# Performance work log

Measured on AMD Instinct MI355X. Metric: run time of the kernel, lower is better.

## Reference

```python
import jax, jax.numpy as jnp
import numpy as np

STRIDES = (8, 16, 32)
H = W = 640
SCORE_T = 0.5
NMS_T = 0.4


def setup_inputs() -> dict:
    key = jax.random.key(0)
    ks = jax.random.split(key, 9)
    feats = [(H // s) * (W // s) for s in STRIDES]  # 6400, 1600, 400
    d = {}
    for i, n in enumerate(feats):
        d[f"score{i}"] = jax.random.normal(ks[i], (1, n, 1), jnp.float32)
        d[f"bbox{i}"] = jax.random.normal(ks[3 + i], (1, n, 4), jnp.float32)
        d[f"kps{i}"] = jax.random.normal(ks[6 + i], (1, n, 10), jnp.float32)
    return d


def _anchors(stride):
    fh, fw = H // stride, W // stride
    yv, xv = jnp.meshgrid(jnp.arange(fh), jnp.arange(fw), indexing="ij")
    return jnp.stack([xv, yv], -1).reshape(-1, 2).astype(jnp.float32) * stride


def _decode(score, bbox, kps, stride):
    pts = _anchors(stride)                      # [N,2]
    s = jax.nn.sigmoid(score[0]).reshape(-1)    # [N]
    d = bbox[0] * stride                        # [N,4]
    x1 = pts[:, 0] - d[:, 0]
    y1 = pts[:, 1] - d[:, 1]
    x2 = pts[:, 0] + d[:, 2]
    y2 = pts[:, 1] + d[:, 3]
    b = jnp.stack([x1, y1, x2, y2], -1)         # [N,4]
    kd = (kps[0] * stride).reshape(-1, 5, 2)    # [N,5,2] (px,py pairs)
    k = (pts[:, None, :] + kd).reshape(-1, 10)  # [N,10]
    return s, b, k


def _iou(b):
    area = (b[:, 2] - b[:, 0]) * (b[:, 3] - b[:, 1])
    lt = jnp.maximum(b[:, None, :2], b[None, :, :2])
    rb = jnp.minimum(b[:, None, 2:], b[None, :, 2:])
    wh = jnp.clip(rb - lt, 0.0)
    inter = wh[..., 0] * wh[..., 1]
    return inter / (area[:, None] + area[None, :] - inter + 1e-9)


def _nms_keep(iou, valid, thresh):
    # greedy NMS on score-sorted boxes: keep i iff no earlier kept j has IoU>thresh
    n = valid.shape[0]
    def body(keep, xs):
        i, row = xs
        suppressed = jnp.any(keep & (row > thresh))
        keep = keep.at[i].set(valid[i] & ~suppressed)
        return keep, None
    keep, _ = jax.lax.scan(body, jnp.zeros(n, bool), (jnp.arange(n), iou))
    return keep


def reference(score0, score1, score2, bbox0, bbox1, bbox2, kps0, kps1, kps2):
    parts = [
        _decode(s, b, k, st)
        for s, b, k, st in zip(
            (score0, score1, score2), (bbox0, bbox1, bbox2), (kps0, kps1, kps2), STRIDES
        )
    ]
    scores = jnp.concatenate([p[0] for p in parts])  # [8400]
    boxes = jnp.concatenate([p[1] for p in parts])   # [8400,4]
    kpss = jnp.concatenate([p[2] for p in parts])    # [8400,10]
    order = jnp.argsort(-scores)                     # score-descending (NMS order)
    scores = scores[order]
    boxes = boxes[order]
    kpss = kpss[order]
    valid = scores > SCORE_T                         # threshold mask
    iou = _iou(jax.lax.stop_gradient(boxes))         # [8400,8400] ~282MB
    keep = _nms_keep(iou, valid, NMS_T)
    m = keep.astype(boxes.dtype)
    # fixed-shape equivalent of dynamic gather: suppressed rows zeroed, keep mask returned
    return boxes * m[:, None], scores * m, kpss * m[:, None], keep
```

## Files before the change

kernel.cpp:

```cpp
#include <hip/hip_runtime.h>
#include <math.h>

#define N_TOT 8400
#define MASK_WORDS 132
#define CAP 32
#define RT 33

typedef unsigned long long u64;

__device__ __forceinline__ unsigned mono_u32(float f) {
    unsigned u = __float_as_uint(f);
    return (u & 0x80000000u) ? ~u : (u | 0x80000000u);
}

__global__ void decode_kernel(const float* __restrict__ score0, const float* __restrict__ bbox0, const float* __restrict__ kps0,
                              const float* __restrict__ score1, const float* __restrict__ bbox1, const float* __restrict__ kps1,
                              const float* __restrict__ score2, const float* __restrict__ bbox2, const float* __restrict__ kps2,
                              float* __restrict__ logit, float* __restrict__ sig,
                              float* __restrict__ box, float* __restrict__ kps,
                              u64* __restrict__ key, int* __restrict__ rank,
                              unsigned int* __restrict__ cnt,
                              u64* __restrict__ validw, u64* __restrict__ rowflag) {
    int i = blockIdx.x * blockDim.x + threadIdx.x;
    if (i >= N_TOT) return;
    if (i < MASK_WORDS) { validw[i] = 0ull; rowflag[i] = 0ull; }
    rank[i] = 0;
    cnt[i] = 0u;
    const float *sc, *bb, *kp;
    int m, F; float s;
    if (i < 6400)      { sc = score0; bb = bbox0; kp = kps0; m = i;        F = 80; s = 8.f;  }
    else if (i < 8000) { sc = score1; bb = bbox1; kp = kps1; m = i - 6400; F = 40; s = 16.f; }
    else               { sc = score2; bb = bbox2; kp = kps2; m = i - 8000; F = 20; s = 32.f; }
    float px = (float)(m % F) * s;
    float py = (float)(m / F) * s;
    float lg = sc[m];
    logit[i] = lg;
    sig[i] = 1.0f / (1.0f + expf(-lg));
    key[i] = ((u64)(~mono_u32(lg)) << 14) | (u64)i;
    float d0 = bb[m*4+0]*s, d1 = bb[m*4+1]*s, d2 = bb[m*4+2]*s, d3 = bb[m*4+3]*s;
    box[i*4+0] = px - d0;
    box[i*4+1] = py - d1;
    box[i*4+2] = px + d2;
    box[i*4+3] = py + d3;
    #pragma unroll
    for (int c = 0; c < 5; ++c) {
        kps[i*10 + 2*c]   = px + kp[m*10 + 2*c]   * s;
        kps[i*10 + 2*c+1] = py + kp[m*10 + 2*c+1] * s;
    }
}

__global__ __launch_bounds__(256) void rank_kernel(const u64* __restrict__ key, int* __restrict__ rank) {
    __shared__ u64 tile[256];
    int i = blockIdx.x * 256 + threadIdx.x;
    int t0 = blockIdx.y * 256;
    u64 ki = (i < N_TOT) ? key[i] : 0ull;
    int j = t0 + threadIdx.x;
    tile[threadIdx.x] = (j < N_TOT) ? key[j] : ~0ull;
    __syncthreads();
    if (i >= N_TOT) return;
    int rk = 0;
    #pragma unroll 8
    for (int k = 0; k < 256; ++k) {
        rk += (tile[k] < ki) ? 1 : 0;
    }
    if (rk) atomicAdd(&rank[i], rk);
}

__global__ void scatter_kernel(const int* __restrict__ rank,
                               const float* __restrict__ logit, const float* __restrict__ sig,
                               const float* __restrict__ box, const float* __restrict__ kps,
                               float* __restrict__ s_logit, float* __restrict__ s_sig,
                               float* __restrict__ s_box, float* __restrict__ s_kps,
                               u64* __restrict__ validw) {
    int i = blockIdx.x * blockDim.x + threadIdx.x;
    if (i >= N_TOT) return;
    int r = rank[i];
    float lg = logit[i];
    s_logit[r] = lg;
    s_sig[r] = sig[i];
    #pragma unroll
    for (int c = 0; c < 4; ++c)  s_box[r*4+c] = box[i*4+c];
    #pragma unroll
    for (int c = 0; c < 10; ++c) s_kps[r*10+c] = kps[i*10+c];
    if (lg > 0.f) atomicOr(&validw[r >> 6], 1ull << (r & 63));
}

__global__ __launch_bounds__(64) void pairs_kernel(const float* __restrict__ s_logit,
                                                   const float* __restrict__ s_box,
                                                   unsigned int* __restrict__ cnt,
                                                   ulonglong2* __restrict__ ent,
                                                   u64* __restrict__ rowflag) {
    int x = blockIdx.x;
    int y = blockIdx.y;
    int rb, cw;
    if (x + y < MASK_WORDS) { rb = x; cw = x + y; }
    else {
        if (y == MASK_WORDS / 2) return;
        rb = x + y - MASK_WORDS; cw = x;
    }
    int tid = threadIdx.x;

    __shared__ float4 cbox[64];
    __shared__ float  carea[64];
    int j0 = cw * 64;
    int j = j0 + tid;
    float4 cb = make_float4(0.f, 0.f, 0.f, 0.f);
    float lgj = -1.f;
    if (j < N_TOT) {
        cb = ((const float4*)s_box)[j];
        lgj = s_logit[j];
    }
    cbox[tid] = cb;
    carea[tid] = (cb.z - cb.x) * (cb.w - cb.y);
    u64 cvalid = __ballot(j < N_TOT && lgj > 0.f);
    __syncthreads();
    if (cvalid == 0ull) return;

    int r = rb * 64 + tid;
    float lgr = (r < N_TOT) ? s_logit[r] : -1.f;
    if (__ballot(lgr > 0.f) == 0ull) return;

    u64 bits = 0ull;
    if (lgr > 0.f) {
        float4 rb4 = ((const float4*)s_box)[r];
        float rarea = (rb4.z - rb4.x) * (rb4.w - rb4.y);
        #pragma unroll 4
        for (int k = 0; k < 64; ++k) {
            float4 c4 = cbox[k];
            float ltx = fmaxf(rb4.x, c4.x);
            float lty = fmaxf(rb4.y, c4.y);
            float rbx = fminf(rb4.z, c4.z);
            float rby = fminf(rb4.w, c4.w);
            float w = fmaxf(rbx - ltx, 0.f);
            float h = fmaxf(rby - lty, 0.f);
            float inter = w * h;
            float iou = inter / (rarea + carea[k] - inter + 1e-9f);
            bits |= (iou > 0.4f) ? (1ull << k) : 0ull;
        }
        u64 m = cvalid;
        if (cw == rb) m &= (tid == 63) ? 0ull : (~0ull << (tid + 1));
        bits &= m;
    }
    if (bits) {
        unsigned idx = atomicAdd(&cnt[r], 1u);
        if (idx < CAP) {
            ulonglong2 e; e.x = bits; e.y = (u64)cw;
            ent[(size_t)r * CAP + idx] = e;
        }
        atomicOr(&rowflag[r >> 6], 1ull << (r & 63));
    }
}

__global__ __launch_bounds__(64) void nms_kernel(const u64* __restrict__ rowflag_g,
                                                 const u64* __restrict__ validw_g,
                                                 const unsigned int* __restrict__ cnt_g,
                                                 const ulonglong2* __restrict__ ent_g,
                                                 u64* __restrict__ keep_words) {
    __shared__ u64 rem_lds[MASK_WORDS];
    __shared__ unsigned short wlist[MASK_WORDS];
    int lane = threadIdx.x;

    u64 rf[3], vw[3];
    #pragma unroll
    for (int s = 0; s < 3; ++s) {
        int w = s * 64 + lane;
        rf[s] = (w < MASK_WORDS) ? rowflag_g[w] : 0ull;
        vw[s] = (w < MASK_WORDS) ? validw_g[w] : 0ull;
        if (w < MASK_WORDS) rem_lds[w] = 0ull;
    }

    int base = 0;
    #pragma unroll
    for (int s = 0; s < 3; ++s) {
        bool nz = rf[s] != 0ull;
        u64 bal = __ballot(nz);
        int pos = __popcll(bal & ((1ull << lane) - 1ull));
        if (nz) wlist[base + pos] = (unsigned short)(s * 64 + lane);
        base += (int)__popcll(bal);
    }
    int n_w = base;
    __syncthreads();

    auto LOADW = [&](int t, int &wd, unsigned &c, ulonglong2 &e0, ulonglong2 &e1, u64 &lb) {
        wd = 0; c = 0u; e0.x = 0ull; e0.y = 0ull; e1.x = 0ull; e1.y = 0ull; lb = 0ull;
        if (t < n_w) {
            wd = (int)wlist[t];
            int row = wd * 64 + lane;
            if (row < N_TOT) {
                c = cnt_g[row];
                if (c > 0u) { e0 = ent_g[(size_t)row * CAP];     if ((int)e0.y == wd) lb |= e0.x; }
                if (c > 1u) { e1 = ent_g[(size_t)row * CAP + 1]; if ((int)e1.y == wd) lb |= e1.x; }
                if (c > 2u) {
                    unsigned cm = min(c, (unsigned)CAP);
                    for (unsigned e = 2; e < cm; ++e) {
                        ulonglong2 g = ent_g[(size_t)row * CAP + e];
                        if ((int)g.y == wd) lb |= g.x;
                    }
                }
            }
        }
    };

    int wA, wB; unsigned cA, cB; ulonglong2 eA0, eA1, eB0, eB1; u64 lbA, lbB;
    LOADW(0, wA, cA, eA0, eA1, lbA);
    LOADW(1, wB, cB, eB0, eB1, lbB);

    for (int t = 0; t < n_w; ++t) {
        int wC; unsigned cC; ulonglong2 eC0, eC1; u64 lbC;
        LOADW(t + 2, wC, cC, eC0, eC1, lbC);

        __syncthreads();
        u64 remw = rem_lds[wA];
        u64 cand = __ballot(cA > 0u) & ~remw;
        if (cand) {
            u64 kept;
            u64 localmask = __ballot(lbA != 0ull) & cand;
            if (localmask == 0ull) {
                kept = cand;
            } else {
                kept = 0ull;
                u64 remw_new = remw;
                u64 pend = cand;
                while (pend) {
                    int b = __builtin_ctzll(pend);
                    pend &= pend - 1ull;
                    if (!((remw_new >> b) & 1ull)) {
                        kept |= 1ull << b;
                        unsigned lo = (unsigned)__builtin_amdgcn_readlane((int)(unsigned)lbA, b);
                        unsigned hi = (unsigned)__builtin_amdgcn_readlane((int)(unsigned)(lbA >> 32), b);
                        remw_new |= ((u64)hi << 32) | (u64)lo;
                        pend &= ~remw_new;
                    }
                }
                if (lane == 0) rem_lds[wA] = remw_new;
            }
            if ((kept >> lane) & 1ull) {
                if (cA > 0u) { int yw = (int)eA0.y; if (yw != wA) atomicOr(&rem_lds[yw], eA0.x); }
                if (cA > 1u) { int yw = (int)eA1.y; if (yw != wA) atomicOr(&rem_lds[yw], eA1.x); }
                if (cA > 2u) {
                    unsigned cm = min(cA, (unsigned)CAP);
                    int row = wA * 64 + lane;
                    for (unsigned e = 2; e < cm; ++e) {
                        ulonglong2 g = ent_g[(size_t)row * CAP + e];
                        int yw = (int)g.y;
                        if (yw != wA) atomicOr(&rem_lds[yw], g.x);
                    }
                }
            }
        }
        wA = wB; cA = cB; eA0 = eB0; eA1 = eB1; lbA = lbB;
        wB = wC; cB = cC; eB0 = eC0; eB1 = eC1; lbB = lbC;
    }

    __syncthreads();
    #pragma unroll
    for (int s = 0; s < 3; ++s) {
        int w = s * 64 + lane;
        if (w < MASK_WORDS) keep_words[w] = vw[s] & ~rem_lds[w];
    }
}

__global__ void output_kernel(const float* __restrict__ s_sig, const float* __restrict__ s_box,
                              const float* __restrict__ s_kps,
                              const u64* __restrict__ keep_words,
                              float* __restrict__ out) {
    int r = blockIdx.x * blockDim.x + threadIdx.x;
    if (r >= N_TOT) return;
    float m = ((keep_words[r >> 6] >> (r & 63)) & 1ull) ? 1.0f : 0.0f;
    float* ob = out;
    float* os = out + 33600;
    float* okp = out + 42000;
    float* om = out + 126000;
    #pragma unroll
    for (int c = 0; c < 4; ++c)  ob[r*4+c] = s_box[r*4+c] * m;
    os[r] = s_sig[r] * m;
    #pragma unroll
    for (int c = 0; c < 10; ++c) okp[r*10+c] = s_kps[r*10+c] * m;
    om[r] = m;
}

extern "C" void kernel_launch(void* const* d_in, const int* in_sizes, int n_in,
                              void* d_out, int out_size, void* d_ws, size_t ws_size,
                              hipStream_t stream) {
    const float *score0, *bbox0, *kps0, *score1, *bbox1, *kps1, *score2, *bbox2, *kps2;
    if (in_sizes[1] == 25600) {
        score0 = (const float*)d_in[0]; bbox0 = (const float*)d_in[1]; kps0 = (const float*)d_in[2];
        score1 = (const float*)d_in[3]; bbox1 = (const float*)d_in[4]; kps1 = (const float*)d_in[5];
        score2 = (const float*)d_in[6]; bbox2 = (const float*)d_in[7]; kps2 = (const float*)d_in[8];
    } else {
        score0 = (const float*)d_in[0]; score1 = (const float*)d_in[1]; score2 = (const float*)d_in[2];
        bbox0  = (const float*)d_in[3]; bbox1  = (const float*)d_in[4]; bbox2  = (const float*)d_in[5];
        kps0   = (const float*)d_in[6]; kps1   = (const float*)d_in[7]; kps2   = (const float*)d_in[8];
    }

    char* ws = (char*)d_ws;
    float* logit   = (float*)(ws + 0);
    float* sig     = (float*)(ws + 33600);
    float* box     = (float*)(ws + 67200);
    float* kps     = (float*)(ws + 201600);
    int*   rank    = (int*)  (ws + 537600);
    float* s_logit = (float*)(ws + 571200);
    float* s_sig   = (float*)(ws + 604800);
    float* s_box   = (float*)(ws + 638400);
    float* s_kps   = (float*)(ws + 772800);
    u64*   keep_words = (u64*)(ws + 1108800);
    u64*   validw     = (u64*)(ws + 1110144);
    u64*   rowflag    = (u64*)(ws + 1111296);
    unsigned int* cnt = (unsigned int*)(ws + 1112448);
    u64*   key        = (u64*)(ws + 1146368);
    ulonglong2*   ent = (ulonglong2*)(ws + 1213568);

    float* out = (float*)d_out;

    decode_kernel<<<(N_TOT + 255) / 256, 256, 0, stream>>>(
        score0, bbox0, kps0, score1, bbox1, kps1, score2, bbox2, kps2,
        logit, sig, box, kps, key, rank, cnt, validw, rowflag);
    rank_kernel<<<dim3(RT, RT), 256, 0, stream>>>(key, rank);
    scatter_kernel<<<33, 256, 0, stream>>>(rank, logit, sig, box, kps,
                                           s_logit, s_sig, s_box, s_kps, validw);
    pairs_kernel<<<dim3(MASK_WORDS, MASK_WORDS / 2 + 1), 64, 0, stream>>>(s_logit, s_box, cnt, ent, rowflag);
    nms_kernel<<<1, 64, 0, stream>>>(rowflag, validw, cnt, ent, keep_words);
    output_kernel<<<33, 256, 0, stream>>>(s_sig, s_box, s_kps, keep_words, out);
}
```

Measured before the change: 113.5 us.

## Fuse the NMS pipeline into one cooperative kernel with grid-wide syncs

Replaces the six separate launches (decode, rank, scatter, pairs, nms, output) with a single cooperative kernel of 256 blocks. Grid syncs separate the stages, the rank and pair tiles are distributed with grid-stride loops, and each wave in the pairs stage gets its own shared-memory slot. The aim is to remove per-launch overhead and the idle gaps between dependent small kernels. In exchange it adds five grid barriers and leaves most blocks idle during the single-wave NMS stage. The old multi-kernel path stays as a fallback if the cooperative launch fails.

```diff
diff --git a/kernel.cpp b/kernel.cpp
--- a/kernel.cpp
+++ b/kernel.cpp
@@ -1,16 +1,306 @@
 #include <hip/hip_runtime.h>
+#include <hip/hip_cooperative_groups.h>
 #include <math.h>
+
+namespace cg = cooperative_groups;
 
 #define N_TOT 8400
 #define MASK_WORDS 132
 #define CAP 32
 #define RT 33
+#define NB 256
+#define NT 256
 
 typedef unsigned long long u64;
 
 __device__ __forceinline__ unsigned mono_u32(float f) {
     unsigned u = __float_as_uint(f);
     return (u & 0x80000000u) ? ~u : (u | 0x80000000u);
+}
+
+#define WS_LOGIT   0
+#define WS_SIG     33600
+#define WS_BOX     67200
+#define WS_KPS     201600
+#define WS_RANK    537600
+#define WS_SLOGIT  571200
+#define WS_SSIG    604800
+#define WS_SBOX    638400
+#define WS_SKPS    772800
+#define WS_KEEP    1108800
+#define WS_VALIDW  1110144
+#define WS_ROWFLAG 1111296
+#define WS_CNT     1112448
+#define WS_KEY     1146368
+#define WS_ENT     1213568
+
+__global__ __launch_bounds__(NT) void fused_kernel(
+        const float* __restrict__ score0, const float* __restrict__ bbox0, const float* __restrict__ kps0,
+        const float* __restrict__ score1, const float* __restrict__ bbox1, const float* __restrict__ kps1,
+        const float* __restrict__ score2, const float* __restrict__ bbox2, const float* __restrict__ kps2,
+        char* __restrict__ ws, float* __restrict__ out) {
+    cg::grid_group grid = cg::this_grid();
+    const int tid = threadIdx.x;
+    const int bid = blockIdx.x;
+    const int gtid = bid * NT + tid;
+
+    float* logit   = (float*)(ws + WS_LOGIT);
+    float* sig     = (float*)(ws + WS_SIG);
+    float* box     = (float*)(ws + WS_BOX);
+    float* kps     = (float*)(ws + WS_KPS);
+    int*   rank    = (int*)  (ws + WS_RANK);
+    float* s_logit = (float*)(ws + WS_SLOGIT);
+    float* s_sig   = (float*)(ws + WS_SSIG);
+    float* s_box   = (float*)(ws + WS_SBOX);
+    float* s_kps   = (float*)(ws + WS_SKPS);
+    u64*   keep_words = (u64*)(ws + WS_KEEP);
+    u64*   validw     = (u64*)(ws + WS_VALIDW);
+    u64*   rowflag    = (u64*)(ws + WS_ROWFLAG);
+    unsigned int* cnt = (unsigned int*)(ws + WS_CNT);
+    u64*   key        = (u64*)(ws + WS_KEY);
+    ulonglong2* ent   = (ulonglong2*)(ws + WS_ENT);
+
+    __shared__ u64 tileK[256];
+    __shared__ float4 cboxS[4][64];
+    __shared__ float  careaS[4][64];
+    __shared__ u64 rem_lds[MASK_WORDS];
+    __shared__ unsigned short wlist[MASK_WORDS];
+
+    if (gtid < N_TOT) {
+        int i = gtid;
+        if (i < MASK_WORDS) { validw[i] = 0ull; rowflag[i] = 0ull; }
+        rank[i] = 0;
+        cnt[i] = 0u;
+        const float *sc, *bb, *kp;
+        int m, F; float s;
+        if (i < 6400)      { sc = score0; bb = bbox0; kp = kps0; m = i;        F = 80; s = 8.f;  }
+        else if (i < 8000) { sc = score1; bb = bbox1; kp = kps1; m = i - 6400; F = 40; s = 16.f; }
+        else               { sc = score2; bb = bbox2; kp = kps2; m = i - 8000; F = 20; s = 32.f; }
+        float px = (float)(m % F) * s;
+        float py = (float)(m / F) * s;
+        float lg = sc[m];
+        logit[i] = lg;
+        sig[i] = 1.0f / (1.0f + expf(-lg));
+        key[i] = ((u64)(~mono_u32(lg)) << 14) | (u64)i;
+        float d0 = bb[m*4+0]*s, d1 = bb[m*4+1]*s, d2 = bb[m*4+2]*s, d3 = bb[m*4+3]*s;
+        box[i*4+0] = px - d0;
+        box[i*4+1] = py - d1;
+        box[i*4+2] = px + d2;
+        box[i*4+3] = py + d3;
+        #pragma unroll
+        for (int c = 0; c < 5; ++c) {
+            kps[i*10 + 2*c]   = px + kp[m*10 + 2*c]   * s;
+            kps[i*10 + 2*c+1] = py + kp[m*10 + 2*c+1] * s;
+        }
+    }
+    grid.sync();
+
+    for (int t = bid; t < RT * RT; t += NB) {
+        int it = t / RT, jt = t - it * RT;
+        __syncthreads();
+        int j = jt * 256 + tid;
+        tileK[tid] = (j < N_TOT) ? key[j] : ~0ull;
+        __syncthreads();
+        int i = it * 256 + tid;
+        if (i < N_TOT) {
+            u64 ki = key[i];
+            int rk = 0;
+            #pragma unroll 8
+            for (int k = 0; k < 256; ++k) rk += (tileK[k] < ki) ? 1 : 0;
+            if (rk) atomicAdd(&rank[i], rk);
+        }
+    }
+    grid.sync();
+
+    if (gtid < N_TOT) {
+        int i = gtid;
+        int r = rank[i];
+        float lg = logit[i];
+        s_logit[r] = lg;
+        s_sig[r] = sig[i];
+        #pragma unroll
+        for (int c = 0; c < 4; ++c)  s_box[r*4+c] = box[i*4+c];
+        #pragma unroll
+        for (int c = 0; c < 10; ++c) s_kps[r*10+c] = kps[i*10+c];
+        if (lg > 0.f) atomicOr(&validw[r >> 6], 1ull << (r & 63));
+    }
+    grid.sync();
+
+    {
+        const int wv = tid >> 6, lane = tid & 63;
+        const int gw = bid * 4 + wv;
+        for (int t = gw; t < 132 * 67; t += NB * 4) {
+            int x = t % 132, y = t / 132;
+            int rb, cw;
+            bool skip = false;
+            if (x + y < MASK_WORDS) { rb = x; cw = x + y; }
+            else if (y == MASK_WORDS / 2) skip = true;
+            else { rb = x + y - MASK_WORDS; cw = x; }
+            if (skip) continue;
+
+            int j = cw * 64 + lane;
+            float4 cb = make_float4(0.f, 0.f, 0.f, 0.f);
+            float lgj = -1.f;
+            if (j < N_TOT) {
+                cb = ((const float4*)s_box)[j];
+                lgj = s_logit[j];
+            }
+            cboxS[wv][lane] = cb;
+            careaS[wv][lane] = (cb.z - cb.x) * (cb.w - cb.y);
+            u64 cvalid = __ballot(j < N_TOT && lgj > 0.f);
+            if (cvalid == 0ull) continue;
+
+            int r = rb * 64 + lane;
+            float lgr = (r < N_TOT) ? s_logit[r] : -1.f;
+            if (__ballot(lgr > 0.f) == 0ull) continue;
+
+            u64 bits = 0ull;
+            if (lgr > 0.f) {
+                float4 rb4 = ((const float4*)s_box)[r];
+                float rarea = (rb4.z - rb4.x) * (rb4.w - rb4.y);
+                #pragma unroll 4
+                for (int k = 0; k < 64; ++k) {
+                    float4 c4 = cboxS[wv][k];
+                    float ltx = fmaxf(rb4.x, c4.x);
+                    float lty = fmaxf(rb4.y, c4.y);
+                    float rbx = fminf(rb4.z, c4.z);
+                    float rby = fminf(rb4.w, c4.w);
+                    float w = fmaxf(rbx - ltx, 0.f);
+                    float h = fmaxf(rby - lty, 0.f);
+                    float inter = w * h;
+                    float iou = inter / (rarea + careaS[wv][k] - inter + 1e-9f);
+                    bits |= (iou > 0.4f) ? (1ull << k) : 0ull;
+                }
+                u64 m = cvalid;
+                if (cw == rb) m &= (lane == 63) ? 0ull : (~0ull << (lane + 1));
+                bits &= m;
+            }
+            if (bits) {
+                unsigned idx = atomicAdd(&cnt[r], 1u);
+                if (idx < CAP) {
+                    ulonglong2 e; e.x = bits; e.y = (u64)cw;
+                    ent[(size_t)r * CAP + idx] = e;
+                }
+                atomicOr(&rowflag[r >> 6], 1ull << (r & 63));
+            }
+        }
+    }
+    grid.sync();
+
+    if (bid == 0 && tid < 64) {
+        int lane = tid;
+        u64 rf[3], vw[3];
+        #pragma unroll
+        for (int s = 0; s < 3; ++s) {
+            int w = s * 64 + lane;
+            rf[s] = (w < MASK_WORDS) ? rowflag[w] : 0ull;
+            vw[s] = (w < MASK_WORDS) ? validw[w] : 0ull;
+            if (w < MASK_WORDS) rem_lds[w] = 0ull;
+        }
+
+        int base = 0;
+        #pragma unroll
+        for (int s = 0; s < 3; ++s) {
+            bool nz = rf[s] != 0ull;
+            u64 bal = __ballot(nz);
+            int pos = __popcll(bal & ((1ull << lane) - 1ull));
+            if (nz) wlist[base + pos] = (unsigned short)(s * 64 + lane);
+            base += (int)__popcll(bal);
+        }
+        int n_w = base;
+
+        auto LOADW = [&](int t, int &wd, unsigned &c, ulonglong2 &e0, ulonglong2 &e1, u64 &lb) {
+            wd = 0; c = 0u; e0.x = 0ull; e0.y = 0ull; e1.x = 0ull; e1.y = 0ull; lb = 0ull;
+            if (t < n_w) {
+                wd = (int)wlist[t];
+                int row = wd * 64 + lane;
+                if (row < N_TOT) {
+                    c = cnt[row];
+                    if (c > 0u) { e0 = ent[(size_t)row * CAP];     if ((int)e0.y == wd) lb |= e0.x; }
+                    if (c > 1u) { e1 = ent[(size_t)row * CAP + 1]; if ((int)e1.y == wd) lb |= e1.x; }
+                    if (c > 2u) {
+                        unsigned cm = min(c, (unsigned)CAP);
+                        for (unsigned e = 2; e < cm; ++e) {
+                            ulonglong2 g = ent[(size_t)row * CAP + e];
+                            if ((int)g.y == wd) lb |= g.x;
+                        }
+                    }
+                }
+            }
+        };
+
+        int wA, wB; unsigned cA, cB; ulonglong2 eA0, eA1, eB0, eB1; u64 lbA, lbB;
+        LOADW(0, wA, cA, eA0, eA1, lbA);
+        LOADW(1, wB, cB, eB0, eB1, lbB);
+
+        for (int t = 0; t < n_w; ++t) {
+            int wC; unsigned cC; ulonglong2 eC0, eC1; u64 lbC;
+            LOADW(t + 2, wC, cC, eC0, eC1, lbC);
+
+            u64 remw = rem_lds[wA];
+            u64 cand = __ballot(cA > 0u) & ~remw;
+            if (cand) {
+                u64 kept;
+                u64 localmask = __ballot(lbA != 0ull) & cand;
+                if (localmask == 0ull) {
+                    kept = cand;
+                } else {
+                    kept = 0ull;
+                    u64 remw_new = remw;
+                    u64 pend = cand;
+                    while (pend) {
+                        int b = __builtin_ctzll(pend);
+                        pend &= pend - 1ull;
+                        if (!((remw_new >> b) & 1ull)) {
+                            kept |= 1ull << b;
+                            unsigned lo = (unsigned)__builtin_amdgcn_readlane((int)(unsigned)lbA, b);
+                            unsigned hi = (unsigned)__builtin_amdgcn_readlane((int)(unsigned)(lbA >> 32), b);
+                            remw_new |= ((u64)hi << 32) | (u64)lo;
+                            pend &= ~remw_new;
+                        }
+                    }
+                    if (lane == 0) rem_lds[wA] = remw_new;
+                }
+                if ((kept >> lane) & 1ull) {
+                    if (cA > 0u) { int yw = (int)eA0.y; if (yw != wA) atomicOr(&rem_lds[yw], eA0.x); }
+                    if (cA > 1u) { int yw = (int)eA1.y; if (yw != wA) atomicOr(&rem_lds[yw], eA1.x); }
+                    if (cA > 2u) {
+                        unsigned cm = min(cA, (unsigned)CAP);
+                        int row = wA * 64 + lane;
+                        for (unsigned e = 2; e < cm; ++e) {
+                            ulonglong2 g = ent[(size_t)row * CAP + e];
+                            int yw = (int)g.y;
+                            if (yw != wA) atomicOr(&rem_lds[yw], g.x);
+                        }
+                    }
+                }
+            }
+            wA = wB; cA = cB; eA0 = eB0; eA1 = eB1; lbA = lbB;
+            wB = wC; cB = cC; eB0 = eC0; eB1 = eC1; lbB = lbC;
+        }
+
+        #pragma unroll
+        for (int s = 0; s < 3; ++s) {
+            int w = s * 64 + lane;
+            if (w < MASK_WORDS) keep_words[w] = vw[s] & ~rem_lds[w];
+        }
+    }
+    grid.sync();
+
+    if (gtid < N_TOT) {
+        int r = gtid;
+        float m = ((keep_words[r >> 6] >> (r & 63)) & 1ull) ? 1.0f : 0.0f;
+        float* ob = out;
+        float* os = out + 33600;
+        float* okp = out + 42000;
+        float* om = out + 126000;
+        #pragma unroll
+        for (int c = 0; c < 4; ++c)  ob[r*4+c] = s_box[r*4+c] * m;
+        os[r] = s_sig[r] * m;
+        #pragma unroll
+        for (int c = 0; c < 10; ++c) okp[r*10+c] = s_kps[r*10+c] * m;
+        om[r] = m;
+    }
 }
 
 __global__ void decode_kernel(const float* __restrict__ score0, const float* __restrict__ bbox0, const float* __restrict__ kps0,
@@ -60,9 +350,7 @@
     if (i >= N_TOT) return;
     int rk = 0;
     #pragma unroll 8
-    for (int k = 0; k < 256; ++k) {
-        rk += (tile[k] < ki) ? 1 : 0;
-    }
+    for (int k = 0; k < 256; ++k) rk += (tile[k] < ki) ? 1 : 0;
     if (rk) atomicAdd(&rank[i], rk);
 }
 
@@ -90,8 +378,7 @@
                                                    unsigned int* __restrict__ cnt,
                                                    ulonglong2* __restrict__ ent,
                                                    u64* __restrict__ rowflag) {
-    int x = blockIdx.x;
-    int y = blockIdx.y;
+    int x = blockIdx.x, y = blockIdx.y;
     int rb, cw;
     if (x + y < MASK_WORDS) { rb = x; cw = x + y; }
     else {
@@ -99,27 +386,20 @@
         rb = x + y - MASK_WORDS; cw = x;
     }
     int tid = threadIdx.x;
-
     __shared__ float4 cbox[64];
     __shared__ float  carea[64];
-    int j0 = cw * 64;
-    int j = j0 + tid;
+    int j = cw * 64 + tid;
     float4 cb = make_float4(0.f, 0.f, 0.f, 0.f);
     float lgj = -1.f;
-    if (j < N_TOT) {
-        cb = ((const float4*)s_box)[j];
-        lgj = s_logit[j];
-    }
+    if (j < N_TOT) { cb = ((const float4*)s_box)[j]; lgj = s_logit[j]; }
     cbox[tid] = cb;
     carea[tid] = (cb.z - cb.x) * (cb.w - cb.y);
     u64 cvalid = __ballot(j < N_TOT && lgj > 0.f);
     __syncthreads();
     if (cvalid == 0ull) return;
-
     int r = rb * 64 + tid;
     float lgr = (r < N_TOT) ? s_logit[r] : -1.f;
     if (__ballot(lgr > 0.f) == 0ull) return;
-
     u64 bits = 0ull;
     if (lgr > 0.f) {
         float4 rb4 = ((const float4*)s_box)[r];
@@ -159,7 +439,6 @@
     __shared__ u64 rem_lds[MASK_WORDS];
     __shared__ unsigned short wlist[MASK_WORDS];
     int lane = threadIdx.x;
-
     u64 rf[3], vw[3];
     #pragma unroll
     for (int s = 0; s < 3; ++s) {
@@ -168,7 +447,6 @@
         vw[s] = (w < MASK_WORDS) ? validw_g[w] : 0ull;
         if (w < MASK_WORDS) rem_lds[w] = 0ull;
     }
-
     int base = 0;
     #pragma unroll
     for (int s = 0; s < 3; ++s) {
@@ -180,7 +458,6 @@
     }
     int n_w = base;
     __syncthreads();
-
     auto LOADW = [&](int t, int &wd, unsigned &c, ulonglong2 &e0, ulonglong2 &e1, u64 &lb) {
         wd = 0; c = 0u; e0.x = 0ull; e0.y = 0ull; e1.x = 0ull; e1.y = 0ull; lb = 0ull;
         if (t < n_w) {
@@ -200,24 +477,20 @@
             }
         }
     };
-
     int wA, wB; unsigned cA, cB; ulonglong2 eA0, eA1, eB0, eB1; u64 lbA, lbB;
     LOADW(0, wA, cA, eA0, eA1, lbA);
     LOADW(1, wB, cB, eB0, eB1, lbB);
-
     for (int t = 0; t < n_w; ++t) {
         int wC; unsigned cC; ulonglong2 eC0, eC1; u64 lbC;
         LOADW(t + 2, wC, cC, eC0, eC1, lbC);
-
         __syncthreads();
         u64 remw = rem_lds[wA];
         u64 cand = __ballot(cA > 0u) & ~remw;
         if (cand) {
             u64 kept;
             u64 localmask = __ballot(lbA != 0ull) & cand;
-            if (localmask == 0ull) {
-                kept = cand;
-            } else {
+            if (localmask == 0ull) kept = cand;
+            else {
                 kept = 0ull;
                 u64 remw_new = remw;
                 u64 pend = cand;
@@ -251,7 +524,6 @@
         wA = wB; cA = cB; eA0 = eB0; eA1 = eB1; lbA = lbB;
         wB = wC; cB = cC; eB0 = eC0; eB1 = eC1; lbB = lbC;
     }
-
     __syncthreads();
     #pragma unroll
     for (int s = 0; s < 3; ++s) {
@@ -294,23 +566,32 @@
     }
 
     char* ws = (char*)d_ws;
-    float* logit   = (float*)(ws + 0);
-    float* sig     = (float*)(ws + 33600);
-    float* box     = (float*)(ws + 67200);
-    float* kps     = (float*)(ws + 201600);
-    int*   rank    = (int*)  (ws + 537600);
-    float* s_logit = (float*)(ws + 571200);
-    float* s_sig   = (float*)(ws + 604800);
-    float* s_box   = (float*)(ws + 638400);
-    float* s_kps   = (float*)(ws + 772800);
-    u64*   keep_words = (u64*)(ws + 1108800);
-    u64*   validw     = (u64*)(ws + 1110144);
-    u64*   rowflag    = (u64*)(ws + 1111296);
-    unsigned int* cnt = (unsigned int*)(ws + 1112448);
-    u64*   key        = (u64*)(ws + 1146368);
-    ulonglong2*   ent = (ulonglong2*)(ws + 1213568);
-
     float* out = (float*)d_out;
+
+    void* args[] = {
+        (void*)&score0, (void*)&bbox0, (void*)&kps0,
+        (void*)&score1, (void*)&bbox1, (void*)&kps1,
+        (void*)&score2, (void*)&bbox2, (void*)&kps2,
+        (void*)&ws, (void*)&out
+    };
+    hipError_t err = hipLaunchCooperativeKernel(fused_kernel, dim3(NB), dim3(NT), args, 0u, stream);
+    if (err == hipSuccess) return;
+
+    float* logit   = (float*)(ws + WS_LOGIT);
+    float* sig     = (float*)(ws + WS_SIG);
+    float* box     = (float*)(ws + WS_BOX);
+    float* kps     = (float*)(ws + WS_KPS);
+    int*   rank    = (int*)  (ws + WS_RANK);
+    float* s_logit = (float*)(ws + WS_SLOGIT);
+    float* s_sig   = (float*)(ws + WS_SSIG);
+    float* s_box   = (float*)(ws + WS_SBOX);
+    float* s_kps   = (float*)(ws + WS_SKPS);
+    u64*   keep_words = (u64*)(ws + WS_KEEP);
+    u64*   validw     = (u64*)(ws + WS_VALIDW);
+    u64*   rowflag    = (u64*)(ws + WS_ROWFLAG);
+    unsigned int* cnt = (unsigned int*)(ws + WS_CNT);
+    u64*   key        = (u64*)(ws + WS_KEY);
+    ulonglong2*   ent = (ulonglong2*)(ws + WS_ENT);
 
     decode_kernel<<<(N_TOT + 255) / 256, 256, 0, stream>>>(
         score0, bbox0, kps0, score1, bbox1, kps1, score2, bbox2, kps2,
```

Result: slower. 260.9 us (+129.9%).

## Fuse six-kernel NMS pipeline into two kernels with last-block NMS tail

Applied to the files above, without the earlier changes.

Collapses decode, rank, scatter into one kernel where each block loads all sort keys into LDS and 16 threads cooperatively compute each element's rank, then write sorted boxes and outputs directly. Pairwise IoU and the serial NMS plus output masking are merged into one persistent-style kernel using a done counter so the last block runs the greedy scan and zeroes suppressed rows. This removes four launches and intermediate global buffers, at the cost of redundant key loading per block (525 blocks × 8400 keys) and a serial tail running on one block.

```diff
diff --git a/kernel.cpp b/kernel.cpp
--- a/kernel.cpp
+++ b/kernel.cpp
@@ -4,7 +4,8 @@
 #define N_TOT 8400
 #define MASK_WORDS 132
 #define CAP 32
-#define RT 33
+#define NBB 256
+#define NBA 525
 
 typedef unsigned long long u64;
 
@@ -13,270 +14,273 @@
     return (u & 0x80000000u) ? ~u : (u | 0x80000000u);
 }
 
-__global__ void decode_kernel(const float* __restrict__ score0, const float* __restrict__ bbox0, const float* __restrict__ kps0,
-                              const float* __restrict__ score1, const float* __restrict__ bbox1, const float* __restrict__ kps1,
-                              const float* __restrict__ score2, const float* __restrict__ bbox2, const float* __restrict__ kps2,
-                              float* __restrict__ logit, float* __restrict__ sig,
-                              float* __restrict__ box, float* __restrict__ kps,
-                              u64* __restrict__ key, int* __restrict__ rank,
-                              unsigned int* __restrict__ cnt,
-                              u64* __restrict__ validw, u64* __restrict__ rowflag) {
-    int i = blockIdx.x * blockDim.x + threadIdx.x;
-    if (i >= N_TOT) return;
-    if (i < MASK_WORDS) { validw[i] = 0ull; rowflag[i] = 0ull; }
-    rank[i] = 0;
-    cnt[i] = 0u;
-    const float *sc, *bb, *kp;
-    int m, F; float s;
-    if (i < 6400)      { sc = score0; bb = bbox0; kp = kps0; m = i;        F = 80; s = 8.f;  }
-    else if (i < 8000) { sc = score1; bb = bbox1; kp = kps1; m = i - 6400; F = 40; s = 16.f; }
-    else               { sc = score2; bb = bbox2; kp = kps2; m = i - 8000; F = 20; s = 32.f; }
-    float px = (float)(m % F) * s;
-    float py = (float)(m / F) * s;
-    float lg = sc[m];
-    logit[i] = lg;
-    sig[i] = 1.0f / (1.0f + expf(-lg));
-    key[i] = ((u64)(~mono_u32(lg)) << 14) | (u64)i;
-    float d0 = bb[m*4+0]*s, d1 = bb[m*4+1]*s, d2 = bb[m*4+2]*s, d3 = bb[m*4+3]*s;
-    box[i*4+0] = px - d0;
-    box[i*4+1] = py - d1;
-    box[i*4+2] = px + d2;
-    box[i*4+3] = py + d3;
-    #pragma unroll
-    for (int c = 0; c < 5; ++c) {
-        kps[i*10 + 2*c]   = px + kp[m*10 + 2*c]   * s;
-        kps[i*10 + 2*c+1] = py + kp[m*10 + 2*c+1] * s;
+#define WS_SLOGIT  0
+#define WS_SBOX    33600
+#define WS_CNT     168000
+#define WS_ROWFLAG 201600
+#define WS_DONE    202656
+#define WS_ENT     202672
+
+__global__ __launch_bounds__(256) void decode_rank_kernel(
+        const float* __restrict__ score0, const float* __restrict__ bbox0, const float* __restrict__ kps0,
+        const float* __restrict__ score1, const float* __restrict__ bbox1, const float* __restrict__ kps1,
+        const float* __restrict__ score2, const float* __restrict__ bbox2, const float* __restrict__ kps2,
+        float* __restrict__ s_logit, float* __restrict__ s_box,
+        unsigned* __restrict__ cnt, u64* __restrict__ rowflag, unsigned* __restrict__ done_ctr,
+        float* __restrict__ out) {
+    __shared__ u64 keyL[N_TOT];
+    const int tid = threadIdx.x;
+    const int gtid = blockIdx.x * 256 + tid;
+
+    if (gtid < N_TOT) cnt[gtid] = 0u;
+    if (gtid < MASK_WORDS) rowflag[gtid] = 0ull;
+    if (gtid == 0) *done_ctr = 0u;
+
+    for (int j = tid; j < N_TOT; j += 256) {
+        const float* sc; int m;
+        if (j < 6400)      { sc = score0; m = j; }
+        else if (j < 8000) { sc = score1; m = j - 6400; }
+        else               { sc = score2; m = j - 8000; }
+        float lg = sc[m];
+        keyL[j] = ((u64)(~mono_u32(lg)) << 14) | (u64)j;
+    }
+    __syncthreads();
+
+    const int i = gtid >> 4;
+    const int sub = tid & 15;
+    u64 ki = keyL[i];
+    int rk = 0;
+    #pragma unroll 7
+    for (int k = 0; k < N_TOT / 16; ++k) {
+        rk += (keyL[sub + (k << 4)] < ki) ? 1 : 0;
+    }
+    rk += __shfl_xor(rk, 1);
+    rk += __shfl_xor(rk, 2);
+    rk += __shfl_xor(rk, 4);
+    rk += __shfl_xor(rk, 8);
+
+    if (sub == 0) {
+        int r = rk;
+        const float *sc, *bb, *kp; int m, F; float s;
+        if (i < 6400)      { sc=score0; bb=bbox0; kp=kps0; m=i;       F=80; s=8.f;  }
+        else if (i < 8000) { sc=score1; bb=bbox1; kp=kps1; m=i-6400;  F=40; s=16.f; }
+        else               { sc=score2; bb=bbox2; kp=kps2; m=i-8000;  F=20; s=32.f; }
+        float px = (float)(m % F) * s;
+        float py = (float)(m / F) * s;
+        float lg = sc[m];
+        s_logit[r] = lg;
+        float d0=bb[m*4+0]*s, d1=bb[m*4+1]*s, d2=bb[m*4+2]*s, d3=bb[m*4+3]*s;
+        float x1 = px - d0, y1 = py - d1, x2 = px + d2, y2 = py + d3;
+        ((float4*)s_box)[r] = make_float4(x1, y1, x2, y2);
+        float* ob  = out;
+        float* os  = out + 33600;
+        float* okp = out + 42000;
+        ob[r*4+0]=x1; ob[r*4+1]=y1; ob[r*4+2]=x2; ob[r*4+3]=y2;
+        os[r] = 1.0f / (1.0f + expf(-lg));
+        #pragma unroll
+        for (int c = 0; c < 5; ++c) {
+            okp[r*10 + 2*c]   = px + kp[m*10 + 2*c]   * s;
+            okp[r*10 + 2*c+1] = py + kp[m*10 + 2*c+1] * s;
+        }
     }
 }
 
-__global__ __launch_bounds__(256) void rank_kernel(const u64* __restrict__ key, int* __restrict__ rank) {
-    __shared__ u64 tile[256];
-    int i = blockIdx.x * 256 + threadIdx.x;
-    int t0 = blockIdx.y * 256;
-    u64 ki = (i < N_TOT) ? key[i] : 0ull;
-    int j = t0 + threadIdx.x;
-    tile[threadIdx.x] = (j < N_TOT) ? key[j] : ~0ull;
-    __syncthreads();
-    if (i >= N_TOT) return;
-    int rk = 0;
-    #pragma unroll 8
-    for (int k = 0; k < 256; ++k) {
-        rk += (tile[k] < ki) ? 1 : 0;
-    }
-    if (rk) atomicAdd(&rank[i], rk);
-}
-
-__global__ void scatter_kernel(const int* __restrict__ rank,
-                               const float* __restrict__ logit, const float* __restrict__ sig,
-                               const float* __restrict__ box, const float* __restrict__ kps,
-                               float* __restrict__ s_logit, float* __restrict__ s_sig,
-                               float* __restrict__ s_box, float* __restrict__ s_kps,
-                               u64* __restrict__ validw) {
-    int i = blockIdx.x * blockDim.x + threadIdx.x;
-    if (i >= N_TOT) return;
-    int r = rank[i];
-    float lg = logit[i];
-    s_logit[r] = lg;
-    s_sig[r] = sig[i];
-    #pragma unroll
-    for (int c = 0; c < 4; ++c)  s_box[r*4+c] = box[i*4+c];
-    #pragma unroll
-    for (int c = 0; c < 10; ++c) s_kps[r*10+c] = kps[i*10+c];
-    if (lg > 0.f) atomicOr(&validw[r >> 6], 1ull << (r & 63));
-}
-
-__global__ __launch_bounds__(64) void pairs_kernel(const float* __restrict__ s_logit,
-                                                   const float* __restrict__ s_box,
-                                                   unsigned int* __restrict__ cnt,
-                                                   ulonglong2* __restrict__ ent,
-                                                   u64* __restrict__ rowflag) {
-    int x = blockIdx.x;
-    int y = blockIdx.y;
-    int rb, cw;
-    if (x + y < MASK_WORDS) { rb = x; cw = x + y; }
-    else {
-        if (y == MASK_WORDS / 2) return;
-        rb = x + y - MASK_WORDS; cw = x;
-    }
-    int tid = threadIdx.x;
-
-    __shared__ float4 cbox[64];
-    __shared__ float  carea[64];
-    int j0 = cw * 64;
-    int j = j0 + tid;
-    float4 cb = make_float4(0.f, 0.f, 0.f, 0.f);
-    float lgj = -1.f;
-    if (j < N_TOT) {
-        cb = ((const float4*)s_box)[j];
-        lgj = s_logit[j];
-    }
-    cbox[tid] = cb;
-    carea[tid] = (cb.z - cb.x) * (cb.w - cb.y);
-    u64 cvalid = __ballot(j < N_TOT && lgj > 0.f);
-    __syncthreads();
-    if (cvalid == 0ull) return;
-
-    int r = rb * 64 + tid;
-    float lgr = (r < N_TOT) ? s_logit[r] : -1.f;
-    if (__ballot(lgr > 0.f) == 0ull) return;
-
-    u64 bits = 0ull;
-    if (lgr > 0.f) {
-        float4 rb4 = ((const float4*)s_box)[r];
-        float rarea = (rb4.z - rb4.x) * (rb4.w - rb4.y);
-        #pragma unroll 4
-        for (int k = 0; k < 64; ++k) {
-            float4 c4 = cbox[k];
-            float ltx = fmaxf(rb4.x, c4.x);
-            float lty = fmaxf(rb4.y, c4.y);
-            float rbx = fminf(rb4.z, c4.z);
-            float rby = fminf(rb4.w, c4.w);
-            float w = fmaxf(rbx - ltx, 0.f);
-            float h = fmaxf(rby - lty, 0.f);
-            float inter = w * h;
-            float iou = inter / (rarea + carea[k] - inter + 1e-9f);
-            bits |= (iou > 0.4f) ? (1ull << k) : 0ull;
-        }
-        u64 m = cvalid;
-        if (cw == rb) m &= (tid == 63) ? 0ull : (~0ull << (tid + 1));
-        bits &= m;
-    }
-    if (bits) {
-        unsigned idx = atomicAdd(&cnt[r], 1u);
-        if (idx < CAP) {
-            ulonglong2 e; e.x = bits; e.y = (u64)cw;
-            ent[(size_t)r * CAP + idx] = e;
-        }
-        atomicOr(&rowflag[r >> 6], 1ull << (r & 63));
-    }
-}
-
-__global__ __launch_bounds__(64) void nms_kernel(const u64* __restrict__ rowflag_g,
-                                                 const u64* __restrict__ validw_g,
-                                                 const unsigned int* __restrict__ cnt_g,
-                                                 const ulonglong2* __restrict__ ent_g,
-                                                 u64* __restrict__ keep_words) {
+__global__ __launch_bounds__(256) void pairs_nms_kernel(
+        const float* __restrict__ s_logit, const float* __restrict__ s_box,
+        unsigned* __restrict__ cnt, ulonglong2* __restrict__ ent,
+        u64* __restrict__ rowflag, unsigned* __restrict__ done_ctr,
+        float* __restrict__ out) {
+    __shared__ float4 cboxS[4][64];
+    __shared__ float  careaS[4][64];
+    __shared__ u64 vw_lds[MASK_WORDS];
     __shared__ u64 rem_lds[MASK_WORDS];
     __shared__ unsigned short wlist[MASK_WORDS];
-    int lane = threadIdx.x;
-
-    u64 rf[3], vw[3];
-    #pragma unroll
-    for (int s = 0; s < 3; ++s) {
-        int w = s * 64 + lane;
-        rf[s] = (w < MASK_WORDS) ? rowflag_g[w] : 0ull;
-        vw[s] = (w < MASK_WORDS) ? validw_g[w] : 0ull;
-        if (w < MASK_WORDS) rem_lds[w] = 0ull;
-    }
-
-    int base = 0;
-    #pragma unroll
-    for (int s = 0; s < 3; ++s) {
-        bool nz = rf[s] != 0ull;
-        u64 bal = __ballot(nz);
-        int pos = __popcll(bal & ((1ull << lane) - 1ull));
-        if (nz) wlist[base + pos] = (unsigned short)(s * 64 + lane);
-        base += (int)__popcll(bal);
-    }
-    int n_w = base;
-    __syncthreads();
-
-    auto LOADW = [&](int t, int &wd, unsigned &c, ulonglong2 &e0, ulonglong2 &e1, u64 &lb) {
-        wd = 0; c = 0u; e0.x = 0ull; e0.y = 0ull; e1.x = 0ull; e1.y = 0ull; lb = 0ull;
-        if (t < n_w) {
-            wd = (int)wlist[t];
-            int row = wd * 64 + lane;
-            if (row < N_TOT) {
-                c = cnt_g[row];
-                if (c > 0u) { e0 = ent_g[(size_t)row * CAP];     if ((int)e0.y == wd) lb |= e0.x; }
-                if (c > 1u) { e1 = ent_g[(size_t)row * CAP + 1]; if ((int)e1.y == wd) lb |= e1.x; }
-                if (c > 2u) {
-                    unsigned cm = min(c, (unsigned)CAP);
-                    for (unsigned e = 2; e < cm; ++e) {
-                        ulonglong2 g = ent_g[(size_t)row * CAP + e];
-                        if ((int)g.y == wd) lb |= g.x;
+    __shared__ int lastF;
+
+    const int tid = threadIdx.x;
+    const int wv = tid >> 6, lane = tid & 63;
+    const int gw = blockIdx.x * 4 + wv;
+
+    for (int t = gw; t < 132 * 67; t += NBB * 4) {
+        int x = t % 132, y = t / 132;
+        int rb, cw;
+        if (x + y < MASK_WORDS) { rb = x; cw = x + y; }
+        else if (y == MASK_WORDS / 2) continue;
+        else { rb = x + y - MASK_WORDS; cw = x; }
+
+        int j = cw * 64 + lane;
+        float4 cb = make_float4(0.f, 0.f, 0.f, 0.f);
+        float lgj = -1.f;
+        if (j < N_TOT) {
+            cb = ((const float4*)s_box)[j];
+            lgj = s_logit[j];
+        }
+        cboxS[wv][lane] = cb;
+        careaS[wv][lane] = (cb.z - cb.x) * (cb.w - cb.y);
+        u64 cvalid = __ballot(j < N_TOT && lgj > 0.f);
+        if (cvalid == 0ull) continue;
+
+        int r = rb * 64 + lane;
+        float lgr = (r < N_TOT) ? s_logit[r] : -1.f;
+        if (__ballot(lgr > 0.f) == 0ull) continue;
+
+        u64 bits = 0ull;
+        if (lgr > 0.f) {
+            float4 rb4 = ((const float4*)s_box)[r];
+            float rarea = (rb4.z - rb4.x) * (rb4.w - rb4.y);
+            #pragma unroll 4
+            for (int k = 0; k < 64; ++k) {
+                float4 c4 = cboxS[wv][k];
+                float ltx = fmaxf(rb4.x, c4.x);
+                float lty = fmaxf(rb4.y, c4.y);
+                float rbx = fminf(rb4.z, c4.z);
+                float rby = fminf(rb4.w, c4.w);
+                float w = fmaxf(rbx - ltx, 0.f);
+                float h = fmaxf(rby - lty, 0.f);
+                float inter = w * h;
+                float iou = inter / (rarea + careaS[wv][k] - inter + 1e-9f);
+                bits |= (iou > 0.4f) ? (1ull << k) : 0ull;
+            }
+            u64 m = cvalid;
+            if (cw == rb) m &= (lane == 63) ? 0ull : (~0ull << (lane + 1));
+            bits &= m;
+        }
+        if (bits) {
+            unsigned idx = atomicAdd(&cnt[r], 1u);
+            if (idx < CAP) {
+                ulonglong2 e; e.x = bits; e.y = (u64)cw;
+                ent[(size_t)r * CAP + idx] = e;
+            }
+            atomicOr(&rowflag[r >> 6], 1ull << (r & 63));
+        }
+    }
+
+    __threadfence();
+    __syncthreads();
+    if (tid == 0) {
+        unsigned p = atomicAdd(done_ctr, 1u);
+        lastF = (p == NBB - 1u) ? 1 : 0;
+    }
+    __syncthreads();
+    if (!lastF) return;
+    __threadfence();
+
+    for (int q = wv * 33; q < wv * 33 + 33; ++q) {
+        int row = q * 64 + lane;
+        float lgq = (row < N_TOT) ? s_logit[row] : -1.f;
+        u64 b = __ballot(lgq > 0.f);
+        if (lane == 0) vw_lds[q] = b;
+    }
+    for (int q = tid; q < MASK_WORDS; q += 256) rem_lds[q] = 0ull;
+    __syncthreads();
+
+    if (wv == 0) {
+        u64 rf[3];
+        #pragma unroll
+        for (int s = 0; s < 3; ++s) {
+            int w = s * 64 + lane;
+            rf[s] = (w < MASK_WORDS) ? rowflag[w] : 0ull;
+        }
+        int base = 0;
+        #pragma unroll
+        for (int s = 0; s < 3; ++s) {
+            bool nz = rf[s] != 0ull;
+            u64 bal = __ballot(nz);
+            int pos = __popcll(bal & ((1ull << lane) - 1ull));
+            if (nz) wlist[base + pos] = (unsigned short)(s * 64 + lane);
+            base += (int)__popcll(bal);
+        }
+        int n_w = base;
+
+        auto LOADW = [&](int t, int &wd, unsigned &c, ulonglong2 &e0, ulonglong2 &e1, u64 &lb) {
+            wd = 0; c = 0u; e0.x = 0ull; e0.y = 0ull; e1.x = 0ull; e1.y = 0ull; lb = 0ull;
+            if (t < n_w) {
+                wd = (int)wlist[t];
+                int row = wd * 64 + lane;
+                if (row < N_TOT) {
+                    c = cnt[row];
+                    if (c > 0u) { e0 = ent[(size_t)row * CAP];     if ((int)e0.y == wd) lb |= e0.x; }
+                    if (c > 1u) { e1 = ent[(size_t)row * CAP + 1]; if ((int)e1.y == wd) lb |= e1.x; }
+                    if (c > 2u) {
+                        unsigned cm = min(c, (unsigned)CAP);
+                        for (unsigned e = 2; e < cm; ++e) {
+                            ulonglong2 g = ent[(size_t)row * CAP + e];
+                            if ((int)g.y == wd) lb |= g.x;
+                        }
                     }
                 }
             }
-        }
-    };
-
-    int wA, wB; unsigned cA, cB; ulonglong2 eA0, eA1, eB0, eB1; u64 lbA, lbB;
-    LOADW(0, wA, cA, eA0, eA1, lbA);
-    LOADW(1, wB, cB, eB0, eB1, lbB);
-
-    for (int t = 0; t < n_w; ++t) {
-        int wC; unsigned cC; ulonglong2 eC0, eC1; u64 lbC;
-        LOADW(t + 2, wC, cC, eC0, eC1, lbC);
-
-        __syncthreads();
-        u64 remw = rem_lds[wA];
-        u64 cand = __ballot(cA > 0u) & ~remw;
-        if (cand) {
-            u64 kept;
-            u64 localmask = __ballot(lbA != 0ull) & cand;
-            if (localmask == 0ull) {
-                kept = cand;
-            } else {
-                kept = 0ull;
-                u64 remw_new = remw;
-                u64 pend = cand;
-                while (pend) {
-                    int b = __builtin_ctzll(pend);
-                    pend &= pend - 1ull;
-                    if (!((remw_new >> b) & 1ull)) {
-                        kept |= 1ull << b;
-                        unsigned lo = (unsigned)__builtin_amdgcn_readlane((int)(unsigned)lbA, b);
-                        unsigned hi = (unsigned)__builtin_amdgcn_readlane((int)(unsigned)(lbA >> 32), b);
-                        remw_new |= ((u64)hi << 32) | (u64)lo;
-                        pend &= ~remw_new;
+        };
+
+        int wA, wB; unsigned cA, cB; ulonglong2 eA0, eA1, eB0, eB1; u64 lbA, lbB;
+        LOADW(0, wA, cA, eA0, eA1, lbA);
+        LOADW(1, wB, cB, eB0, eB1, lbB);
+
+        for (int t = 0; t < n_w; ++t) {
+            int wC; unsigned cC; ulonglong2 eC0, eC1; u64 lbC;
+            LOADW(t + 2, wC, cC, eC0, eC1, lbC);
+
+            u64 remw = rem_lds[wA];
+            u64 cand = __ballot(cA > 0u) & ~remw;
+            if (cand) {
+                u64 kept;
+                u64 localmask = __ballot(lbA != 0ull) & cand;
+                if (localmask == 0ull) {
+                    kept = cand;
+                } else {
+                    kept = 0ull;
+                    u64 remw_new = remw;
+                    u64 pend = cand;
+                    while (pend) {
+                        int b = __builtin_ctzll(pend);
+                        pend &= pend - 1ull;
+                        if (!((remw_new >> b) & 1ull)) {
+                            kept |= 1ull << b;
+                            unsigned lo = (unsigned)__builtin_amdgcn_readlane((int)(unsigned)lbA, b);
+                            unsigned hi = (unsigned)__builtin_amdgcn_readlane((int)(unsigned)(lbA >> 32), b);
+                            remw_new |= ((u64)hi << 32) | (u64)lo;
+                            pend &= ~remw_new;
+                        }
+                    }
+                    if (lane == 0) rem_lds[wA] = remw_new;
+                }
+                if ((kept >> lane) & 1ull) {
+                    if (cA > 0u) { int yw = (int)eA0.y; if (yw != wA) atomicOr(&rem_lds[yw], eA0.x); }
+                    if (cA > 1u) { int yw = (int)eA1.y; if (yw != wA) atomicOr(&rem_lds[yw], eA1.x); }
+                    if (cA > 2u) {
+                        unsigned cm = min(cA, (unsigned)CAP);
+                        int row = wA * 64 + lane;
+                        for (unsigned e = 2; e < cm; ++e) {
+                            ulonglong2 g = ent[(size_t)row * CAP + e];
+                            int yw = (int)g.y;
+                            if (yw != wA) atomicOr(&rem_lds[yw], g.x);
+                        }
                     }
                 }
-                if (lane == 0) rem_lds[wA] = remw_new;
-            }
-            if ((kept >> lane) & 1ull) {
-                if (cA > 0u) { int yw = (int)eA0.y; if (yw != wA) atomicOr(&rem_lds[yw], eA0.x); }
-                if (cA > 1u) { int yw = (int)eA1.y; if (yw != wA) atomicOr(&rem_lds[yw], eA1.x); }
-                if (cA > 2u) {
-                    unsigned cm = min(cA, (unsigned)CAP);
-                    int row = wA * 64 + lane;
-                    for (unsigned e = 2; e < cm; ++e) {
-                        ulonglong2 g = ent_g[(size_t)row * CAP + e];
-                        int yw = (int)g.y;
-                        if (yw != wA) atomicOr(&rem_lds[yw], g.x);
-                    }
-                }
-            }
-        }
-        wA = wB; cA = cB; eA0 = eB0; eA1 = eB1; lbA = lbB;
-        wB = wC; cB = cC; eB0 = eC0; eB1 = eC1; lbB = lbC;
-    }
-
-    __syncthreads();
-    #pragma unroll
-    for (int s = 0; s < 3; ++s) {
-        int w = s * 64 + lane;
-        if (w < MASK_WORDS) keep_words[w] = vw[s] & ~rem_lds[w];
-    }
-}
-
-__global__ void output_kernel(const float* __restrict__ s_sig, const float* __restrict__ s_box,
-                              const float* __restrict__ s_kps,
-                              const u64* __restrict__ keep_words,
-                              float* __restrict__ out) {
-    int r = blockIdx.x * blockDim.x + threadIdx.x;
-    if (r >= N_TOT) return;
-    float m = ((keep_words[r >> 6] >> (r & 63)) & 1ull) ? 1.0f : 0.0f;
-    float* ob = out;
-    float* os = out + 33600;
-    float* okp = out + 42000;
-    float* om = out + 126000;
-    #pragma unroll
-    for (int c = 0; c < 4; ++c)  ob[r*4+c] = s_box[r*4+c] * m;
-    os[r] = s_sig[r] * m;
-    #pragma unroll
-    for (int c = 0; c < 10; ++c) okp[r*10+c] = s_kps[r*10+c] * m;
-    om[r] = m;
+            }
+            wA = wB; cA = cB; eA0 = eB0; eA1 = eB1; lbA = lbB;
+            wB = wC; cB = cC; eB0 = eC0; eB1 = eC1; lbB = lbC;
+        }
+    }
+    __syncthreads();
+
+    {
+        float* ob  = out;
+        float* os  = out + 33600;
+        float* okp = out + 42000;
+        float* om  = out + 126000;
+        for (int r = tid; r < N_TOT; r += 256) {
+            u64 kw = vw_lds[r >> 6] & ~rem_lds[r >> 6];
+            bool keep = (kw >> (r & 63)) & 1ull;
+            om[r] = keep ? 1.0f : 0.0f;
+            if (!keep) {
+                ((float4*)ob)[r] = make_float4(0.f, 0.f, 0.f, 0.f);
+                os[r] = 0.f;
+                #pragma unroll
+                for (int c = 0; c < 10; ++c) okp[r*10 + c] = 0.f;
+            }
+        }
+    }
 }
 
 extern "C" void kernel_launch(void* const* d_in, const int* in_sizes, int n_in,
@@ -294,31 +298,17 @@
     }
 
     char* ws = (char*)d_ws;
-    float* logit   = (float*)(ws + 0);
-    float* sig     = (float*)(ws + 33600);
-    float* box     = (float*)(ws + 67200);
-    float* kps     = (float*)(ws + 201600);
-    int*   rank    = (int*)  (ws + 537600);
-    float* s_logit = (float*)(ws + 571200);
-    float* s_sig   = (float*)(ws + 604800);
-    float* s_box   = (float*)(ws + 638400);
-    float* s_kps   = (float*)(ws + 772800);
-    u64*   keep_words = (u64*)(ws + 1108800);
-    u64*   validw     = (u64*)(ws + 1110144);
-    u64*   rowflag    = (u64*)(ws + 1111296);
-    unsigned int* cnt = (unsigned int*)(ws + 1112448);
-    u64*   key        = (u64*)(ws + 1146368);
-    ulonglong2*   ent = (ulonglong2*)(ws + 1213568);
-
+    float* s_logit      = (float*)(ws + WS_SLOGIT);
+    float* s_box        = (float*)(ws + WS_SBOX);
+    unsigned* cnt       = (unsigned*)(ws + WS_CNT);
+    u64* rowflag        = (u64*)(ws + WS_ROWFLAG);
+    unsigned* done_ctr  = (unsigned*)(ws + WS_DONE);
+    ulonglong2* ent     = (ulonglong2*)(ws + WS_ENT);
     float* out = (float*)d_out;
 
-    decode_kernel<<<(N_TOT + 255) / 256, 256, 0, stream>>>(
+    decode_rank_kernel<<<NBA, 256, 0, stream>>>(
         score0, bbox0, kps0, score1, bbox1, kps1, score2, bbox2, kps2,
-        logit, sig, box, kps, key, rank, cnt, validw, rowflag);
-    rank_kernel<<<dim3(RT, RT), 256, 0, stream>>>(key, rank);
-    scatter_kernel<<<33, 256, 0, stream>>>(rank, logit, sig, box, kps,
-                                           s_logit, s_sig, s_box, s_kps, validw);
-    pairs_kernel<<<dim3(MASK_WORDS, MASK_WORDS / 2 + 1), 64, 0, stream>>>(s_logit, s_box, cnt, ent, rowflag);
-    nms_kernel<<<1, 64, 0, stream>>>(rowflag, validw, cnt, ent, keep_words);
-    output_kernel<<<33, 256, 0, stream>>>(s_sig, s_box, s_kps, keep_words, out);
+        s_logit, s_box, cnt, rowflag, done_ctr, out);
+    pairs_nms_kernel<<<NBB, 256, 0, stream>>>(
+        s_logit, s_box, cnt, ent, rowflag, done_ctr, out);
 }
```

Measured after the change: 152.6 us. 1.34x slower.
